# Kernel tuning notes

Measured on AMD Instinct MI355X. Metric: run time of the kernel, lower is better.

Reference implementation:

```python
import jax, jax.numpy as jnp
import numpy as np

B, T, S, H, V = 4, 512, 1024, 768, 50257

def setup_inputs() -> dict:
    key = jax.random.key(0)
    k1, k2, k3, k4, k5, k6 = jax.random.split(key, 6)
    input_ids_to_copy = jax.random.randint(k1, (B, S), 0, V)
    cross_attentions = jax.random.uniform(k2, (B, T, S), dtype=jnp.float32)
    # normalize like attention weights
    cross_attentions = cross_attentions / jnp.sum(cross_attentions, axis=-1, keepdims=True)
    src_hidden_states = jax.random.normal(k3, (B, S, H), dtype=jnp.float32)
    tgt_hidden_states = jax.random.normal(k4, (B, T, H), dtype=jnp.float32)
    # p_gen_head = Linear(2H, 1) + Sigmoid
    W_pgen = jax.random.normal(k5, (2 * H, 1), dtype=jnp.float32) * (1.0 / np.sqrt(2 * H))
    b_pgen = jnp.zeros((1,), dtype=jnp.float32)
    return {
        "input_ids_to_copy": input_ids_to_copy,
        "cross_attentions": cross_attentions,
        "src_hidden_states": src_hidden_states,
        "tgt_hidden_states": tgt_hidden_states,
        "W_pgen": W_pgen,
        "b_pgen": b_pgen,
    }

def _copy_logits(attn_bts, ids_bs, vocab_size):
    # logits[b,t,v] = sum_s attn[b,t,s] * (ids[b,s] == v)
    # Efficient scatter-add over source positions instead of one-hot + matmul.
    def per_batch(attn_ts, ids_s):
        # attn_ts: [T,S], ids_s: [S] -> segment_sum over S -> [V,T] -> [T,V]
        return jax.ops.segment_sum(attn_ts.T, ids_s, num_segments=vocab_size).T
    return jax.vmap(per_batch)(attn_bts, ids_bs)

def reference(input_ids_to_copy, cross_attentions, src_hidden_states,
              tgt_hidden_states, W_pgen, b_pgen):
    # context_vectors: [B,T,H]
    context_vectors = jnp.einsum('bts,bsh->bth', cross_attentions, src_hidden_states)
    total_states = jnp.concatenate((context_vectors, tgt_hidden_states), axis=-1)  # [B,T,2H]
    p_gen = jax.nn.sigmoid(total_states @ W_pgen + b_pgen)  # [B,T,1]
    logits = _copy_logits(cross_attentions, input_ids_to_copy, V)  # [B,T,V]
    return (p_gen, logits)
```

## Files before the change

kernel.cpp:

```cpp
#include <hip/hip_runtime.h>
#include <hip/hip_bf16.h>
#include <math.h>

#define BB 4
#define TT 512
#define SS 1024
#define HH 768
#define VV 50257
#define NW 1571
#define NWP 1600

typedef float vfloat4 __attribute__((ext_vector_type(4)));

__global__ __launch_bounds__(256) void proj_kernel(
    const float* __restrict__ src, const float* __restrict__ tgt,
    const float* __restrict__ W, const float* __restrict__ bptr,
    float* __restrict__ src_proj, float* __restrict__ tgt_proj)
{
    const int wave = threadIdx.x >> 6;
    const int lane = threadIdx.x & 63;
    const int row  = blockIdx.x * 4 + wave;

    const float* vec;
    const float* w;
    if (row < BB * SS) { vec = src + (size_t)row * HH;            w = W; }
    else               { vec = tgt + (size_t)(row - BB*SS) * HH;  w = W + HH; }
    const float4* v4 = (const float4*)vec;
    const float4* w4 = (const float4*)w;

    float acc = 0.f;
#pragma unroll
    for (int k = 0; k < 3; ++k) {
        float4 a = v4[k * 64 + lane];
        float4 b = w4[k * 64 + lane];
        acc += a.x * b.x + a.y * b.y + a.z * b.z + a.w * b.w;
    }
#pragma unroll
    for (int off = 32; off > 0; off >>= 1) acc += __shfl_down(acc, off);
    if (lane == 0) {
        if (row < BB * SS) src_proj[row] = acc;
        else               tgt_proj[row - BB * SS] = acc + bptr[0];
    }
}

__global__ __launch_bounds__(256) void batch_setup(
    const int* __restrict__ ids,
    unsigned* __restrict__ bm_g,
    unsigned* __restrict__ pre_g,
    unsigned short* __restrict__ rank_g)
{
    __shared__ unsigned bm[NW];
    __shared__ unsigned pre[NW];
    __shared__ unsigned scan[256];
    const int b = blockIdx.x, tid = threadIdx.x;

    for (int i = tid; i < NW; i += 256) bm[i] = 0u;
    __syncthreads();
    const int* idb = ids + b * SS;
    for (int s = tid; s < SS; s += 256) {
        const int v = idb[s];
        atomicOr(&bm[v >> 5], 1u << (v & 31));
    }
    __syncthreads();

    unsigned cnt[7];
    unsigned local = 0;
    const int w0 = tid * 7;
#pragma unroll
    for (int k = 0; k < 7; ++k) {
        const int w = w0 + k;
        cnt[k] = local;
        local += (w < NW) ? (unsigned)__popc(bm[w]) : 0u;
    }
    scan[tid] = local;
    __syncthreads();
    for (int off = 1; off < 256; off <<= 1) {
        const unsigned mine = scan[tid];
        const unsigned add  = (tid >= off) ? scan[tid - off] : 0u;
        __syncthreads();
        scan[tid] = mine + add;
        __syncthreads();
    }
    const unsigned excl = (tid > 0) ? scan[tid - 1] : 0u;
#pragma unroll
    for (int k = 0; k < 7; ++k) {
        const int w = w0 + k;
        if (w < NW) {
            const unsigned p = excl + cnt[k];
            pre[w] = p;
            pre_g[b * NWP + w] = p;
            bm_g[b * NWP + w]  = bm[w];
        }
    }
    __syncthreads();
    for (int s = tid; s < SS; s += 256) {
        const int v = idb[s];
        const unsigned w = (unsigned)v >> 5, bit = (unsigned)v & 31u;
        const unsigned r = pre[w] + (unsigned)__popc(bm[w] & ((1u << bit) - 1u));
        rank_g[b * SS + s] = (unsigned short)r;
    }
}

__device__ __forceinline__ float lut1(int v, const unsigned* bm,
                                      const unsigned* pre, const float* vals)
{
    const unsigned w = bm[v >> 5];
    const unsigned bit = (unsigned)v & 31u;
    if ((w >> bit) & 1u)
        return vals[pre[v >> 5] + (unsigned)__popc(w & ((1u << bit) - 1u))];
    return 0.f;
}

__global__ __launch_bounds__(256) void row_kernel(
    const float* __restrict__ attn,
    const float* __restrict__ src_proj,
    const float* __restrict__ tgt_proj,
    const unsigned* __restrict__ bm_g,
    const unsigned* __restrict__ pre_g,
    const unsigned short* __restrict__ rank_g,
    float* __restrict__ out)
{
    __shared__ unsigned bm[NW];
    __shared__ unsigned pre[NW];
    __shared__ float vals[SS];
    __shared__ float wsum[4];

    const int row = blockIdx.x;
    const int b   = row >> 9;
    const int tid = threadIdx.x;

    for (int i = tid; i < NW; i += 256) { bm[i] = bm_g[b*NWP+i]; pre[i] = pre_g[b*NWP+i]; }
    ((float4*)vals)[tid] = make_float4(0.f, 0.f, 0.f, 0.f);
    __syncthreads();

    const float4*  a4p = (const float4*)(attn + (size_t)row * SS);
    const float4*  sp4 = (const float4*)(src_proj + b * SS);
    const ushort4* r4p = (const ushort4*)(rank_g + b * SS);
    const float4  a = a4p[tid];
    const float4  p = sp4[tid];
    const ushort4 r = r4p[tid];
    atomicAdd(&vals[r.x], a.x);
    atomicAdd(&vals[r.y], a.y);
    atomicAdd(&vals[r.z], a.z);
    atomicAdd(&vals[r.w], a.w);
    float acc = a.x * p.x + a.y * p.y + a.z * p.z + a.w * p.w;
#pragma unroll
    for (int off = 32; off > 0; off >>= 1) acc += __shfl_down(acc, off);
    if ((tid & 63) == 0) wsum[tid >> 6] = acc;
    __syncthreads();
    if (tid == 0) {
        const float x = wsum[0] + wsum[1] + wsum[2] + wsum[3] + tgt_proj[row];
        out[row] = 1.f / (1.f + expf(-x));
    }

    float* logits = out + (BB * TT) + (size_t)row * VV;
    const int head = (int)(((16u - (unsigned)((uintptr_t)logits & 15u)) & 15u) >> 2);
    if (tid < head)
        __builtin_nontemporal_store(lut1(tid, bm, pre, vals), logits + tid);

    const int n4 = (VV - head) >> 2;
    vfloat4* p4 = (vfloat4*)(logits + head);
    for (int i = tid; i < n4; i += 256) {
        const int v0 = head + (i << 2);
        vfloat4 o = {0.f, 0.f, 0.f, 0.f};
        const unsigned w  = bm[v0 >> 5];
        const unsigned sh = (unsigned)v0 & 31u;
        unsigned nib;
        if (sh <= 28u) {
            nib = (w >> sh) & 0xFu;
        } else {
            const unsigned hi = bm[(v0 >> 5) + 1];
            nib = ((w >> sh) | (hi << (32u - sh))) & 0xFu;
        }
        if (nib) {
            o.x = lut1(v0,     bm, pre, vals);
            o.y = lut1(v0 + 1, bm, pre, vals);
            o.z = lut1(v0 + 2, bm, pre, vals);
            o.w = lut1(v0 + 3, bm, pre, vals);
        }
        __builtin_nontemporal_store(o, p4 + i);
    }
    const int done = head + (n4 << 2);
    for (int v = done + tid; v < VV; v += 256)
        __builtin_nontemporal_store(lut1(v, bm, pre, vals), logits + v);
}

extern "C" void kernel_launch(void* const* d_in, const int* in_sizes, int n_in,
                              void* d_out, int out_size, void* d_ws, size_t ws_size,
                              hipStream_t stream) {
    const int*   ids  = (const int*)d_in[0];
    const float* attn = (const float*)d_in[1];
    const float* src  = (const float*)d_in[2];
    const float* tgt  = (const float*)d_in[3];
    const float* W    = (const float*)d_in[4];
    const float* bp   = (const float*)d_in[5];

    float* out = (float*)d_out;

    float*          src_proj = (float*)d_ws;
    float*          tgt_proj = src_proj + BB * SS;
    unsigned*       bm_g     = (unsigned*)(tgt_proj + BB * TT);
    unsigned*       pre_g    = bm_g + BB * NWP;
    unsigned short* rank_g   = (unsigned short*)(pre_g + BB * NWP);

    proj_kernel<<<(BB * SS + BB * TT) / 4, 256, 0, stream>>>(
        src, tgt, W, bp, src_proj, tgt_proj);
    batch_setup<<<BB, 256, 0, stream>>>(ids, bm_g, pre_g, rank_g);
    row_kernel<<<BB * TT, 256, 0, stream>>>(
        attn, src_proj, tgt_proj, bm_g, pre_g, rank_g, out);
}
```

Baseline: 486.4 us.

## Merge projection and batch setup kernels; use regular stores for logits

Combines the p_gen projection kernel and the per-batch bitmap/rank setup kernel into one launch, with the block index deciding which role a block plays. This saves one kernel launch and lets the small setup blocks run alongside the projection blocks. Separately, the logits output writes switch from nontemporal stores to ordinary stores, which changes how the large output write interacts with the cache.

```diff
diff --git a/kernel.cpp b/kernel.cpp
--- a/kernel.cpp
+++ b/kernel.cpp
@@ -9,50 +9,50 @@
 #define VV 50257
 #define NW 1571
 #define NWP 1600
-
-typedef float vfloat4 __attribute__((ext_vector_type(4)));
-
-__global__ __launch_bounds__(256) void proj_kernel(
+#define NPROJ 1536
+
+__global__ __launch_bounds__(256) void prep_kernel(
     const float* __restrict__ src, const float* __restrict__ tgt,
     const float* __restrict__ W, const float* __restrict__ bptr,
-    float* __restrict__ src_proj, float* __restrict__ tgt_proj)
-{
-    const int wave = threadIdx.x >> 6;
-    const int lane = threadIdx.x & 63;
-    const int row  = blockIdx.x * 4 + wave;
-
-    const float* vec;
-    const float* w;
-    if (row < BB * SS) { vec = src + (size_t)row * HH;            w = W; }
-    else               { vec = tgt + (size_t)(row - BB*SS) * HH;  w = W + HH; }
-    const float4* v4 = (const float4*)vec;
-    const float4* w4 = (const float4*)w;
-
-    float acc = 0.f;
-#pragma unroll
-    for (int k = 0; k < 3; ++k) {
-        float4 a = v4[k * 64 + lane];
-        float4 b = w4[k * 64 + lane];
-        acc += a.x * b.x + a.y * b.y + a.z * b.z + a.w * b.w;
-    }
-#pragma unroll
-    for (int off = 32; off > 0; off >>= 1) acc += __shfl_down(acc, off);
-    if (lane == 0) {
-        if (row < BB * SS) src_proj[row] = acc;
-        else               tgt_proj[row - BB * SS] = acc + bptr[0];
-    }
-}
-
-__global__ __launch_bounds__(256) void batch_setup(
     const int* __restrict__ ids,
-    unsigned* __restrict__ bm_g,
-    unsigned* __restrict__ pre_g,
+    float* __restrict__ src_proj, float* __restrict__ tgt_proj,
+    unsigned* __restrict__ bm_g, unsigned* __restrict__ pre_g,
     unsigned short* __restrict__ rank_g)
 {
     __shared__ unsigned bm[NW];
     __shared__ unsigned pre[NW];
     __shared__ unsigned scan[256];
-    const int b = blockIdx.x, tid = threadIdx.x;
+    const int tid = threadIdx.x;
+
+    if (blockIdx.x < NPROJ) {
+        const int wave = tid >> 6;
+        const int lane = tid & 63;
+        const int row  = blockIdx.x * 4 + wave;
+
+        const float* vec;
+        const float* w;
+        if (row < BB * SS) { vec = src + (size_t)row * HH;            w = W; }
+        else               { vec = tgt + (size_t)(row - BB*SS) * HH;  w = W + HH; }
+        const float4* v4 = (const float4*)vec;
+        const float4* w4 = (const float4*)w;
+
+        float acc = 0.f;
+#pragma unroll
+        for (int k = 0; k < 3; ++k) {
+            float4 a = v4[k * 64 + lane];
+            float4 b = w4[k * 64 + lane];
+            acc += a.x * b.x + a.y * b.y + a.z * b.z + a.w * b.w;
+        }
+#pragma unroll
+        for (int off = 32; off > 0; off >>= 1) acc += __shfl_down(acc, off);
+        if (lane == 0) {
+            if (row < BB * SS) src_proj[row] = acc;
+            else               tgt_proj[row - BB * SS] = acc + bptr[0];
+        }
+        return;
+    }
+
+    const int b = blockIdx.x - NPROJ;
 
     for (int i = tid; i < NW; i += 256) bm[i] = 0u;
     __syncthreads();
@@ -155,14 +155,13 @@
 
     float* logits = out + (BB * TT) + (size_t)row * VV;
     const int head = (int)(((16u - (unsigned)((uintptr_t)logits & 15u)) & 15u) >> 2);
-    if (tid < head)
-        __builtin_nontemporal_store(lut1(tid, bm, pre, vals), logits + tid);
+    if (tid < head) logits[tid] = lut1(tid, bm, pre, vals);
 
     const int n4 = (VV - head) >> 2;
-    vfloat4* p4 = (vfloat4*)(logits + head);
+    float4* p4 = (float4*)(logits + head);
     for (int i = tid; i < n4; i += 256) {
         const int v0 = head + (i << 2);
-        vfloat4 o = {0.f, 0.f, 0.f, 0.f};
+        float4 o = make_float4(0.f, 0.f, 0.f, 0.f);
         const unsigned w  = bm[v0 >> 5];
         const unsigned sh = (unsigned)v0 & 31u;
         unsigned nib;
@@ -178,11 +177,11 @@
             o.z = lut1(v0 + 2, bm, pre, vals);
             o.w = lut1(v0 + 3, bm, pre, vals);
         }
-        __builtin_nontemporal_store(o, p4 + i);
+        p4[i] = o;
     }
     const int done = head + (n4 << 2);
     for (int v = done + tid; v < VV; v += 256)
-        __builtin_nontemporal_store(lut1(v, bm, pre, vals), logits + v);
+        logits[v] = lut1(v, bm, pre, vals);
 }
 
 extern "C" void kernel_launch(void* const* d_in, const int* in_sizes, int n_in,
@@ -203,9 +202,8 @@
     unsigned*       pre_g    = bm_g + BB * NWP;
     unsigned short* rank_g   = (unsigned short*)(pre_g + BB * NWP);
 
-    proj_kernel<<<(BB * SS + BB * TT) / 4, 256, 0, stream>>>(
-        src, tgt, W, bp, src_proj, tgt_proj);
-    batch_setup<<<BB, 256, 0, stream>>>(ids, bm_g, pre_g, rank_g);
+    prep_kernel<<<NPROJ + BB, 256, 0, stream>>>(
+        src, tgt, W, bp, ids, src_proj, tgt_proj, bm_g, pre_g, rank_g);
     row_kernel<<<BB * TT, 256, 0, stream>>>(
         attn, src_proj, tgt_proj, bm_g, pre_g, rank_g, out);
 }
```

After: 463.2 us (median of 2 runs). -4.8%, faster.
